# Performance work log

Measured on AMD Instinct MI355X. Metric: run time of the kernel, lower is better.

The kernel has to match this reference:

```python
import jax, jax.numpy as jnp
import numpy as np

B, C, N = 2, 29, 8192
S, K = 1024, 16  # npoint, nsample
D = C + 3


def fps(xyz_t, npoint):
    # xyz_t: [B, N, 3] -> indices [B, npoint] (furthest point sampling, starts at idx 0)
    b, n, _ = xyz_t.shape

    def step(carry, _):
        dists, farthest = carry  # [B,N], [B]
        centroid = jnp.take_along_axis(xyz_t, farthest[:, None, None], axis=1)  # [B,1,3]
        d = jnp.sum((xyz_t - centroid) ** 2, axis=-1)  # [B,N]
        dists = jnp.minimum(dists, d)
        nxt = jnp.argmax(dists, axis=-1)
        return (dists, nxt), farthest

    init = (jnp.full((b, n), 1e10, xyz_t.dtype), jnp.zeros((b,), jnp.int32))
    _, idx = jax.lax.scan(step, init, None, length=npoint)
    return jnp.transpose(idx)  # [B, npoint]


def knn_self(pts, k):
    # pts: [B, S, 3] -> k nearest neighbor indices within the same set, [B, S, k]
    sq = jnp.sum(pts * pts, axis=-1)
    d2 = sq[:, :, None] + sq[:, None, :] - 2.0 * jnp.einsum('bic,bjc->bij', pts, pts)
    _, idx = jax.lax.top_k(-d2, k)
    return idx


def group(arr, idx):
    # arr: [B, C, N], idx: [B, S, K] -> [B, C, S, K]
    return jax.vmap(lambda a, i: a[:, i])(arr, idx)


def squeeze_2x2(x):
    # RealNVP alt-order squeeze: [n, c, h, w] -> [n, 4c, h/2, w/2]
    tl = x[:, :, 0::2, 0::2]
    br = x[:, :, 1::2, 1::2]
    tr = x[:, :, 0::2, 1::2]
    bl = x[:, :, 1::2, 0::2]
    return jnp.concatenate([tl, br, tr, bl], axis=1)


def conv2d(x, w):
    return jax.lax.conv_general_dilated(
        x, w, window_strides=(1, 1), padding='VALID',
        dimension_numbers=('NCHW', 'OIHW', 'NCHW'))


def setup_inputs() -> dict:
    key = jax.random.key(0)
    ks = jax.random.split(key, 6)
    return {
        'xyz': jax.random.normal(ks[0], (B, 3, N), jnp.float32),
        'feats': jax.random.normal(ks[1], (B, C, N), jnp.float32),
        'w0': jax.random.normal(ks[2], (64, 2 * D * 4, 3, 3), jnp.float32) * 0.02,
        'w1': jax.random.normal(ks[3], (64, 64, 3, 3), jnp.float32) * 0.02,
        'w2': jax.random.normal(ks[4], (128, 64, 3, 3), jnp.float32) * 0.02,
        'w3': jax.random.normal(ks[5], (128, 128, 2, 2), jnp.float32) * 0.02,
    }


def reference(xyz, feats, w0, w1, w2, w3):
    b, c, n = feats.shape
    xyz_t = jnp.transpose(xyz, (0, 2, 1))  # [B,N,3]
    fps_idx = fps(xyz_t, S)  # [B,S]
    new_xyz = jnp.take_along_axis(xyz, fps_idx[:, None, :], axis=2)  # [B,3,S]
    new_xyz_t = jnp.transpose(new_xyz, (0, 2, 1))  # [B,S,3]
    idx = knn_self(new_xyz_t, K)  # [B,S,K], values in [0,S)

    pos_grouped = group(new_xyz, idx)  # [B,3,S,K]
    feats_grouped = group(feats, idx)  # [B,C,S,K] (indices < S, as in original)
    pos_diff = pos_grouped - new_xyz[:, :, :, None]
    fg = jnp.concatenate([pos_diff, feats_grouped], axis=1)  # [B,D,S,K]

    # pairwise outer-product features; second half ([fg;1] x [fg;1] upper block) is all ones
    outer = jnp.einsum('bdsi,bdsj->bdsij', fg, fg)  # [B,D,S,K,K]
    mat = jnp.concatenate([outer, jnp.ones_like(outer)], axis=1)  # [B,2D,S,K,K]
    mat = jnp.transpose(mat, (0, 2, 1, 3, 4)).reshape(b * S, 2 * D, K, K)
    mat = squeeze_2x2(mat)  # [B*S, 8D, K/2, K/2]

    for w in (w0, w1, w2, w3):  # use_bn=False -> Identity bns; spatial 8->6->4->2->1
        mat = jax.nn.relu(conv2d(mat, w))

    new_points = jnp.transpose(mat.reshape(b, S, -1), (0, 2, 1))  # [B,128,S]
    return new_xyz, new_points, fps_idx
```

## Files before the change

kernel.cpp:

```cpp
#include <hip/hip_runtime.h>
#include <hip/hip_bf16.h>

#pragma clang fp contract(off)

#define NPTS 8192
#define NS   1024
#define NB   2
#define NC   29
#define NK   16


__global__ __launch_bounds__(256) void prep_kernel(
    const float* __restrict__ w0, const float* __restrict__ w1,
    const float* __restrict__ w2, const float* __restrict__ w3,
    float* __restrict__ w0t, float* __restrict__ w1t,
    float* __restrict__ w2t, float* __restrict__ w3t,
    float* __restrict__ bias0)
{
    int i = blockIdx.x * 256 + threadIdx.x;
    int n = gridDim.x * 256;
    for (int e = i; e < 73728; e += n) {
        int o = e & 63, r = e >> 6, tap = r % 9, ic2 = r / 9;
        int ic = ((ic2 >> 5) << 6) + (ic2 & 31);
        w0t[e] = w0[(o * 256 + ic) * 9 + tap];
    }
    for (int e = i; e < 36864; e += n) {
        int o = e & 63, r = e >> 6, tap = r % 9, ic = r / 9;
        w1t[e] = w1[(o * 64 + ic) * 9 + tap];
    }
    for (int e = i; e < 73728; e += n) {
        int o = e & 127, r = e >> 7, tap = r % 9, ic = r / 9;
        w2t[e] = w2[(o * 64 + ic) * 9 + tap];
    }
    for (int e = i; e < 65536; e += n) {
        int o = e & 127, r = e >> 7, tap = r & 3, ic = r >> 2;
        w3t[e] = w3[(o * 128 + ic) * 4 + tap];
    }
    if (i < 64) {
        float sum = 0.0f;
        for (int q = 0; q < 4; ++q)
            for (int c = 0; c < 32; ++c)
                for (int t = 0; t < 9; ++t)
                    sum += w0[(i * 256 + q * 64 + 32 + c) * 9 + t];
        bias0[i] = sum;
    }
}

__device__ __forceinline__ float wave_max_nonneg(float x) {
    int v = __float_as_int(x);
    int t;
    t = __builtin_amdgcn_update_dpp(0, v, 0x111, 0xf, 0xf, true);
    v = __float_as_int(fmaxf(__int_as_float(v), __int_as_float(t)));
    t = __builtin_amdgcn_update_dpp(0, v, 0x112, 0xf, 0xf, true);
    v = __float_as_int(fmaxf(__int_as_float(v), __int_as_float(t)));
    t = __builtin_amdgcn_update_dpp(0, v, 0x114, 0xf, 0xf, true);
    v = __float_as_int(fmaxf(__int_as_float(v), __int_as_float(t)));
    t = __builtin_amdgcn_update_dpp(0, v, 0x118, 0xf, 0xf, true);
    v = __float_as_int(fmaxf(__int_as_float(v), __int_as_float(t)));
    t = __builtin_amdgcn_update_dpp(0, v, 0x142, 0xa, 0xf, true);
    v = __float_as_int(fmaxf(__int_as_float(v), __int_as_float(t)));
    t = __builtin_amdgcn_update_dpp(0, v, 0x143, 0xc, 0xf, true);
    v = __float_as_int(fmaxf(__int_as_float(v), __int_as_float(t)));
    return __int_as_float(__builtin_amdgcn_readlane(v, 63));
}

__global__ __launch_bounds__(1024) void fps_kernel(
    const float* __restrict__ xyz,
    float* __restrict__ nx_ws, float* __restrict__ out)
{
    int b = blockIdx.x;
    int tid = threadIdx.x;
    const float* X = xyz + b * 3 * NPTS;

    __shared__ unsigned s_max[2];
    __shared__ int s_gi[2];
    __shared__ int s_idx[NS];

    float px[8], py[8], pz[8], dist[8];
#pragma unroll
    for (int i = 0; i < 8; ++i) {
        int gi = i * 1024 + tid;
        px[i] = X[gi];
        py[i] = X[NPTS + gi];
        pz[i] = X[2 * NPTS + gi];
        dist[i] = 1e10f;
    }

    float* out_fps = out + 268288 + b * NS;
    if (tid == 0) {
        s_idx[0] = 0; out_fps[0] = 0.0f;
        s_max[0] = 0u; s_max[1] = 0u;
        s_gi[0] = 0x7fffffff; s_gi[1] = 0x7fffffff;
    }
    __syncthreads();

    float cx = X[0], cy = X[NPTS], cz = X[2 * NPTS];
    int lane = tid & 63;

    for (int it = 1; it < NS; ++it) {
        int par = it & 1;
#pragma unroll
        for (int i = 0; i < 8; ++i) {
            float dx = px[i] - cx, dy = py[i] - cy, dz = pz[i] - cz;
            float d = (dx * dx + dy * dy) + dz * dz;
            dist[i] = fminf(dist[i], d);
        }
        float m0 = fmaxf(dist[0], dist[1]);
        float m1 = fmaxf(dist[2], dist[3]);
        float m2 = fmaxf(dist[4], dist[5]);
        float m3 = fmaxf(dist[6], dist[7]);
        float m4 = fmaxf(m0, m1);
        float m5 = fmaxf(m2, m3);
        float bv = fmaxf(m4, m5);
        float wm = wave_max_nonneg(bv);
        if (lane == 0) atomicMax(&s_max[par], __float_as_uint(wm));
        __syncthreads();
        float gbv = __uint_as_float(s_max[par]);
        if (tid == 0) { s_max[par ^ 1] = 0u; s_gi[par ^ 1] = 0x7fffffff; }
        if (bv == gbv) {
            int gi = 0;
#pragma unroll
            for (int i = 7; i >= 0; --i)
                if (dist[i] == gbv) gi = (i << 10) + tid;
            atomicMin(&s_gi[par], gi);
        }
        __syncthreads();
        int idx = s_gi[par];
        if (tid == 0) { out_fps[it] = (float)idx; s_idx[it] = idx; }
        cx = X[idx]; cy = X[NPTS + idx]; cz = X[2 * NPTS + idx];
    }
    __syncthreads();
    {
        int j = s_idx[tid];
        float x = X[j], y = X[NPTS + j], z = X[2 * NPTS + j];
        nx_ws[(b * 3 + 0) * NS + tid] = x; out[(b * 3 + 0) * NS + tid] = x;
        nx_ws[(b * 3 + 1) * NS + tid] = y; out[(b * 3 + 1) * NS + tid] = y;
        nx_ws[(b * 3 + 2) * NS + tid] = z; out[(b * 3 + 2) * NS + tid] = z;
    }
}

__global__ __launch_bounds__(256) void knn_kernel(
    const float* __restrict__ nx_ws, int* __restrict__ knn_ws)
{
    int q = blockIdx.x * 4 + (threadIdx.x >> 6);
    int lane = threadIdx.x & 63;
    int b = q >> 10, s = q & 1023;
    const float* P = nx_ws + b * 3 * NS;
    float qx = P[s], qy = P[NS + s], qz = P[2 * NS + s];
    float sqq = (qx * qx + qy * qy) + qz * qz;
    int base_j = lane * 16;
    float d2[16];
    {
        const float4* x4 = (const float4*)(P + base_j);
        const float4* y4 = (const float4*)(P + NS + base_j);
        const float4* z4 = (const float4*)(P + 2 * NS + base_j);
#pragma unroll
        for (int t = 0; t < 4; ++t) {
            float4 xv = x4[t], yv = y4[t], zv = z4[t];
            float xs[4] = { xv.x, xv.y, xv.z, xv.w };
            float ys[4] = { yv.x, yv.y, yv.z, yv.w };
            float zs[4] = { zv.x, zv.y, zv.z, zv.w };
#pragma unroll
            for (int e = 0; e < 4; ++e) {
                float xj = xs[e], yj = ys[e], zj = zs[e];
                float sqj = (xj * xj + yj * yj) + zj * zj;
                float dot = (qx * xj + qy * yj) + qz * zj;
                d2[t * 4 + e] = (sqq + sqj) - 2.0f * dot;
            }
        }
    }
    for (int r = 0; r < NK; ++r) {
        float lv = 3.0e38f; int li = 0;
#pragma unroll
        for (int i = 0; i < 16; ++i) { if (d2[i] < lv) { lv = d2[i]; li = i; } }
        int gj = base_j + li;
#pragma unroll
        for (int off = 32; off > 0; off >>= 1) {
            float ov = __shfl_xor(lv, off, 64);
            int   oj = __shfl_xor(gj, off, 64);
            if (ov < lv || (ov == lv && oj < gj)) { lv = ov; gj = oj; }
        }
        if (lane == 0) knn_ws[q * NK + r] = gj;
        if ((gj >> 4) == lane) {
            int li2 = gj & 15;
#pragma unroll
            for (int i = 0; i < 16; ++i) if (i == li2) d2[i] = 3.0e38f;
        }
    }
}

template<int GODD>
__device__ __forceinline__ void conv0_accum(
    const float* __restrict__ x0r, const float* __restrict__ wbase, float acc[9])
{
    for (int ic2 = 0; ic2 < 128; ++ic2) {
        const float4* x4 = (const float4*)(x0r + ic2 * 64);
        float rr[32];
#pragma unroll
        for (int j = 0; j < 4; ++j) {
            float4 t0 = x4[j * 2], t1 = x4[j * 2 + 1];
            rr[j*8+0]=t0.x; rr[j*8+1]=t0.y; rr[j*8+2]=t0.z; rr[j*8+3]=t0.w;
            rr[j*8+4]=t1.x; rr[j*8+5]=t1.y; rr[j*8+6]=t1.z; rr[j*8+7]=t1.w;
        }
        float w[9];
#pragma unroll
        for (int t = 0; t < 9; ++t) w[t] = wbase[(ic2 * 9 + t) * 64];
#pragma unroll
        for (int pp = 0; pp < 9; ++pp) {
            const int ly = GODD ? (pp < 3 ? 0 : 1) : (pp < 6 ? 0 : 1);
            const int xx = GODD ? (pp < 3 ? pp + 3 : pp - 3) : (pp < 6 ? pp : pp - 6);
#pragma unroll
            for (int ky = 0; ky < 3; ++ky)
#pragma unroll
                for (int kx = 0; kx < 3; ++kx)
                    acc[pp] = __builtin_fmaf(w[ky * 3 + kx], rr[(ly + ky) * 8 + xx + kx], acc[pp]);
        }
    }
}

__global__ __launch_bounds__(256) void conv_kernel(
    const float* __restrict__ feats, const float* __restrict__ nx_ws,
    const int* __restrict__ knn_ws,
    const float* __restrict__ w0t, const float* __restrict__ bias0,
    const float* __restrict__ w1t, const float* __restrict__ w2t,
    const float* __restrict__ w3t, float* __restrict__ out)
{
    __shared__ float s_fg[512];
    __shared__ int   s_ni[16];
    __shared__ float s_x0[8192];
    __shared__ float s_a1[64 * 36];
    __shared__ float s_a2[64 * 16];
    __shared__ float s_a3[128 * 4];

    int bs = blockIdx.x, b = bs >> 10, s = bs & 1023;
    int tid = threadIdx.x;
    if (tid < 16) s_ni[tid] = knn_ws[bs * NK + tid];
    __syncthreads();
    const float* P = nx_ws + b * 3 * NS;
#pragma unroll
    for (int e = tid; e < 512; e += 256) {
        int d = e >> 4, k = e & 15; int j = s_ni[k];
        float v = (d < 3) ? (P[d * NS + j] - P[d * NS + s])
                          : feats[(b * NC + (d - 3)) * NPTS + j];
        s_fg[e] = v;
    }
    __syncthreads();
    for (int e = tid; e < 8192; e += 256) {
        int ic2 = e >> 6, pos = e & 63, u = pos >> 3, v = pos & 7;
        int q = ic2 >> 5, ch = ic2 & 31;
        int ro = q & 1, co = ((q + 1) >> 1) & 1;
        s_x0[e] = s_fg[ch * 16 + 2 * u + ro] * s_fg[ch * 16 + 2 * v + co];
    }
    __syncthreads();

    int o = tid & 63, g = tid >> 6;
    {
        int r0 = g + (g >> 1);
        float acc[9];
        float bz = bias0[o];
#pragma unroll
        for (int p = 0; p < 9; ++p) acc[p] = bz;
        const float* x0r = s_x0 + r0 * 8;
        const float* wb = w0t + o;
        if (g & 1) conv0_accum<1>(x0r, wb, acc);
        else       conv0_accum<0>(x0r, wb, acc);
#pragma unroll
        for (int pp = 0; pp < 9; ++pp) s_a1[o * 36 + g * 9 + pp] = fmaxf(acc[pp], 0.0f);
    }
    __syncthreads();
    {
        float a[4] = {0, 0, 0, 0};
        const float* wb = w1t + o;
        for (int ic = 0; ic < 64; ++ic) {
            const float2* ar2 = (const float2*)(s_a1 + ic * 36 + g * 6);
            float r[18];
#pragma unroll
            for (int t = 0; t < 9; ++t) { float2 tv = ar2[t]; r[t*2] = tv.x; r[t*2+1] = tv.y; }
            float w[9];
#pragma unroll
            for (int t = 0; t < 9; ++t) w[t] = wb[(ic * 9 + t) * 64];
#pragma unroll
            for (int x = 0; x < 4; ++x)
#pragma unroll
                for (int ky = 0; ky < 3; ++ky)
#pragma unroll
                    for (int kx = 0; kx < 3; ++kx)
                        a[x] = __builtin_fmaf(w[ky * 3 + kx], r[ky * 6 + x + kx], a[x]);
        }
#pragma unroll
        for (int x = 0; x < 4; ++x) s_a2[o * 16 + g * 4 + x] = fmaxf(a[x], 0.0f);
    }
    __syncthreads();
    {
        int o2 = tid & 127, g2 = tid >> 7;
        float a[2] = {0, 0};
        const float* wb = w2t + o2;
        for (int ic = 0; ic < 64; ++ic) {
            const float4* ar4 = (const float4*)(s_a2 + ic * 16 + g2 * 4);
            float r[12];
#pragma unroll
            for (int t = 0; t < 3; ++t) { float4 tv = ar4[t]; r[t*4]=tv.x; r[t*4+1]=tv.y; r[t*4+2]=tv.z; r[t*4+3]=tv.w; }
            float w[9];
#pragma unroll
            for (int t = 0; t < 9; ++t) w[t] = wb[(ic * 9 + t) * 128];
#pragma unroll
            for (int x = 0; x < 2; ++x)
#pragma unroll
                for (int ky = 0; ky < 3; ++ky)
#pragma unroll
                    for (int kx = 0; kx < 3; ++kx)
                        a[x] = __builtin_fmaf(w[ky * 3 + kx], r[ky * 4 + x + kx], a[x]);
        }
#pragma unroll
        for (int x = 0; x < 2; ++x) s_a3[o2 * 4 + g2 * 2 + x] = fmaxf(a[x], 0.0f);
    }
    __syncthreads();
    if (tid < 128) {
        float acc = 0.0f;
        const float* wb = w3t + tid;
        for (int ic = 0; ic < 128; ++ic) {
            float4 av = *(const float4*)(s_a3 + ic * 4);
            float wa = wb[(ic * 4 + 0) * 128];
            float wbv = wb[(ic * 4 + 1) * 128];
            float wc = wb[(ic * 4 + 2) * 128];
            float wd = wb[(ic * 4 + 3) * 128];
            acc = __builtin_fmaf(wa, av.x, acc);
            acc = __builtin_fmaf(wbv, av.y, acc);
            acc = __builtin_fmaf(wc, av.z, acc);
            acc = __builtin_fmaf(wd, av.w, acc);
        }
        out[6144 + (b * 128 + tid) * NS + s] = fmaxf(acc, 0.0f);
    }
}

extern "C" void kernel_launch(void* const* d_in, const int* in_sizes, int n_in,
                              void* d_out, int out_size, void* d_ws, size_t ws_size,
                              hipStream_t stream) {
    const float* xyz   = (const float*)d_in[0];
    const float* feats = (const float*)d_in[1];
    const float* w0    = (const float*)d_in[2];
    const float* w1    = (const float*)d_in[3];
    const float* w2    = (const float*)d_in[4];
    const float* w3    = (const float*)d_in[5];
    float* out = (float*)d_out;

    char* ws = (char*)d_ws;
    float* nx_ws  = (float*)(ws + 8192);
    int*   knn_ws = (int*)(ws + 32768);
    float* w0t    = (float*)(ws + 163840);
    float* bias0  = (float*)(ws + 458752);
    float* w1t    = (float*)(ws + 459008);
    float* w2t    = (float*)(ws + 606464);
    float* w3t    = (float*)(ws + 901376);

    prep_kernel<<<128, 256, 0, stream>>>(w0, w1, w2, w3, w0t, w1t, w2t, w3t, bias0);
    fps_kernel<<<NB, 1024, 0, stream>>>(xyz, nx_ws, out);
    knn_kernel<<<(NB * NS) / 4, 256, 0, stream>>>(nx_ws, knn_ws);
    conv_kernel<<<NB * NS, 256, 0, stream>>>(feats, nx_ws, knn_ws, w0t, bias0, w1t, w2t, w3t, out);
}
```

Before: 1.447 ms.

## Restructure FPS with packed 64-bit argmax key and single barrier per iteration

The furthest-point-sampling kernel now uses 256 threads, each holding 32 points as float2 vectors, where it used 1024 threads with 8 points each. The two-phase max-then-min-index reduction, which needed two barriers per iteration, is replaced by one 64-bit atomicMax on a key packing the distance with the inverted index. A per-iteration slot array removes the need to reset shared state. This targets barrier and atomic latency in the serial 1023-step loop. The cost is more per-thread work and higher register pressure.

```diff
diff --git a/kernel.cpp b/kernel.cpp
--- a/kernel.cpp
+++ b/kernel.cpp
@@ -64,78 +64,82 @@
     return __int_as_float(__builtin_amdgcn_readlane(v, 63));
 }
 
-__global__ __launch_bounds__(1024) void fps_kernel(
+typedef float v2f __attribute__((ext_vector_type(2)));
+
+__global__ __launch_bounds__(256, 1) void fps_kernel(
     const float* __restrict__ xyz,
     float* __restrict__ nx_ws, float* __restrict__ out)
 {
     int b = blockIdx.x;
     int tid = threadIdx.x;
+    int lane = tid & 63;
     const float* X = xyz + b * 3 * NPTS;
 
-    __shared__ unsigned s_max[2];
-    __shared__ int s_gi[2];
-    __shared__ int s_idx[NS];
-
-    float px[8], py[8], pz[8], dist[8];
-#pragma unroll
-    for (int i = 0; i < 8; ++i) {
-        int gi = i * 1024 + tid;
-        px[i] = X[gi];
-        py[i] = X[NPTS + gi];
-        pz[i] = X[2 * NPTS + gi];
-        dist[i] = 1e10f;
+    __shared__ unsigned long long s_key[NS];
+
+    v2f px[16], py[16], pz[16], dist[16];
+
+    for (int i = tid; i < NS; i += 256) s_key[i] = 0ull;
+    if (tid == 0) s_key[0] = 0xFFFFFFFFull;
+
+#pragma unroll
+    for (int i = 0; i < 16; ++i) {
+        int g2 = i * 512 + tid * 2;
+        px[i] = *(const v2f*)(X + g2);
+        py[i] = *(const v2f*)(X + NPTS + g2);
+        pz[i] = *(const v2f*)(X + 2 * NPTS + g2);
+        dist[i] = (v2f){1e10f, 1e10f};
+    }
+    __syncthreads();
+
+    float cx = X[0], cy = X[NPTS], cz = X[2 * NPTS];
+
+    for (int it = 1; it < NS; ++it) {
+        v2f c2x = {cx, cx}, c2y = {cy, cy}, c2z = {cz, cz};
+#pragma unroll
+        for (int i = 0; i < 16; ++i) {
+            v2f dx = px[i] - c2x, dy = py[i] - c2y, dz = pz[i] - c2z;
+            v2f d = (dx * dx + dy * dy) + dz * dz;
+            v2f dd = dist[i];
+            dd.x = fminf(dd.x, d.x);
+            dd.y = fminf(dd.y, d.y);
+            dist[i] = dd;
+        }
+        float t16[16];
+#pragma unroll
+        for (int i = 0; i < 16; ++i) t16[i] = fmaxf(dist[i].x, dist[i].y);
+        float t8[8];
+#pragma unroll
+        for (int i = 0; i < 8; ++i) t8[i] = fmaxf(t16[2 * i], t16[2 * i + 1]);
+        float t4[4];
+#pragma unroll
+        for (int i = 0; i < 4; ++i) t4[i] = fmaxf(t8[2 * i], t8[2 * i + 1]);
+        float bv = fmaxf(fmaxf(t4[0], t4[1]), fmaxf(t4[2], t4[3]));
+        float wm = wave_max_nonneg(bv);
+        if (bv == wm) {
+            int gi = 0;
+#pragma unroll
+            for (int i = 15; i >= 0; --i) {
+                if (dist[i].y == wm) gi = i * 512 + tid * 2 + 1;
+                if (dist[i].x == wm) gi = i * 512 + tid * 2;
+            }
+            unsigned long long key =
+                ((unsigned long long)__float_as_uint(wm) << 32) | (unsigned)(~gi);
+            atomicMax(&s_key[it], key);
+        }
+        __syncthreads();
+        int idx = (int)(~(unsigned)s_key[it]);
+        cx = X[idx]; cy = X[NPTS + idx]; cz = X[2 * NPTS + idx];
     }
 
     float* out_fps = out + 268288 + b * NS;
-    if (tid == 0) {
-        s_idx[0] = 0; out_fps[0] = 0.0f;
-        s_max[0] = 0u; s_max[1] = 0u;
-        s_gi[0] = 0x7fffffff; s_gi[1] = 0x7fffffff;
-    }
-    __syncthreads();
-
-    float cx = X[0], cy = X[NPTS], cz = X[2 * NPTS];
-    int lane = tid & 63;
-
-    for (int it = 1; it < NS; ++it) {
-        int par = it & 1;
-#pragma unroll
-        for (int i = 0; i < 8; ++i) {
-            float dx = px[i] - cx, dy = py[i] - cy, dz = pz[i] - cz;
-            float d = (dx * dx + dy * dy) + dz * dz;
-            dist[i] = fminf(dist[i], d);
-        }
-        float m0 = fmaxf(dist[0], dist[1]);
-        float m1 = fmaxf(dist[2], dist[3]);
-        float m2 = fmaxf(dist[4], dist[5]);
-        float m3 = fmaxf(dist[6], dist[7]);
-        float m4 = fmaxf(m0, m1);
-        float m5 = fmaxf(m2, m3);
-        float bv = fmaxf(m4, m5);
-        float wm = wave_max_nonneg(bv);
-        if (lane == 0) atomicMax(&s_max[par], __float_as_uint(wm));
-        __syncthreads();
-        float gbv = __uint_as_float(s_max[par]);
-        if (tid == 0) { s_max[par ^ 1] = 0u; s_gi[par ^ 1] = 0x7fffffff; }
-        if (bv == gbv) {
-            int gi = 0;
-#pragma unroll
-            for (int i = 7; i >= 0; --i)
-                if (dist[i] == gbv) gi = (i << 10) + tid;
-            atomicMin(&s_gi[par], gi);
-        }
-        __syncthreads();
-        int idx = s_gi[par];
-        if (tid == 0) { out_fps[it] = (float)idx; s_idx[it] = idx; }
-        cx = X[idx]; cy = X[NPTS + idx]; cz = X[2 * NPTS + idx];
-    }
-    __syncthreads();
-    {
-        int j = s_idx[tid];
+    for (int i = tid; i < NS; i += 256) {
+        int j = (int)(~(unsigned)s_key[i]);
+        out_fps[i] = (float)j;
         float x = X[j], y = X[NPTS + j], z = X[2 * NPTS + j];
-        nx_ws[(b * 3 + 0) * NS + tid] = x; out[(b * 3 + 0) * NS + tid] = x;
-        nx_ws[(b * 3 + 1) * NS + tid] = y; out[(b * 3 + 1) * NS + tid] = y;
-        nx_ws[(b * 3 + 2) * NS + tid] = z; out[(b * 3 + 2) * NS + tid] = z;
+        nx_ws[(b * 3 + 0) * NS + i] = x; out[(b * 3 + 0) * NS + i] = x;
+        nx_ws[(b * 3 + 1) * NS + i] = y; out[(b * 3 + 1) * NS + i] = y;
+        nx_ws[(b * 3 + 2) * NS + i] = z; out[(b * 3 + 2) * NS + i] = z;
     }
 }
 
@@ -354,7 +358,7 @@
     float* w3t    = (float*)(ws + 901376);
 
     prep_kernel<<<128, 256, 0, stream>>>(w0, w1, w2, w3, w0t, w1t, w2t, w3t, bias0);
-    fps_kernel<<<NB, 1024, 0, stream>>>(xyz, nx_ws, out);
+    fps_kernel<<<NB, 256, 0, stream>>>(xyz, nx_ws, out);
     knn_kernel<<<(NB * NS) / 4, 256, 0, stream>>>(nx_ws, knn_ws);
     conv_kernel<<<NB * NS, 256, 0, stream>>>(feats, nx_ws, knn_ws, w0t, bias0, w1t, w2t, w3t, out);
 }
```

Result: slower. 1.720 ms (+18.9%).

## Fuse FPS argmax into single packed 64-bit atomic, halving barriers per iteration

Applied to the files above, without the earlier changes.

Replaces the two-phase block argmax in the FPS loop (atomicMax on the value, barrier, atomicMin on the index, barrier) with a single 64-bit atomicMax on a key packing the distance bits and the inverted index. Each iteration writes into its own shared slot, so no reset is needed and only one __syncthreads remains per step. The final index array is recovered from the keys afterwards. This halves barrier count on the serial 1023-iteration critical path, at the cost of 64-bit LDS atomics, where every wave's candidate lanes now contend on the shared slot.

```diff
diff --git a/kernel.cpp b/kernel.cpp
--- a/kernel.cpp
+++ b/kernel.cpp
@@ -72,9 +72,7 @@
     int tid = threadIdx.x;
     const float* X = xyz + b * 3 * NPTS;
 
-    __shared__ unsigned s_max[2];
-    __shared__ int s_gi[2];
-    __shared__ int s_idx[NS];
+    __shared__ unsigned long long s_key[NS];
 
     float px[8], py[8], pz[8], dist[8];
 #pragma unroll
@@ -85,20 +83,18 @@
         pz[i] = X[2 * NPTS + gi];
         dist[i] = 1e10f;
     }
-
-    float* out_fps = out + 268288 + b * NS;
-    if (tid == 0) {
-        s_idx[0] = 0; out_fps[0] = 0.0f;
-        s_max[0] = 0u; s_max[1] = 0u;
-        s_gi[0] = 0x7fffffff; s_gi[1] = 0x7fffffff;
-    }
+#pragma unroll
+    for (int i = 0; i < 8; ++i) {
+        asm volatile("" : "+v"(px[i]), "+v"(py[i]), "+v"(pz[i]));
+    }
+
+    s_key[tid] = 0ull;
+    if (tid == 0) s_key[0] = 0xFFFFFFFFull;
     __syncthreads();
 
     float cx = X[0], cy = X[NPTS], cz = X[2 * NPTS];
-    int lane = tid & 63;
 
     for (int it = 1; it < NS; ++it) {
-        int par = it & 1;
 #pragma unroll
         for (int i = 0; i < 8; ++i) {
             float dx = px[i] - cx, dy = py[i] - cy, dz = pz[i] - cz;
@@ -109,29 +105,26 @@
         float m1 = fmaxf(dist[2], dist[3]);
         float m2 = fmaxf(dist[4], dist[5]);
         float m3 = fmaxf(dist[6], dist[7]);
-        float m4 = fmaxf(m0, m1);
-        float m5 = fmaxf(m2, m3);
-        float bv = fmaxf(m4, m5);
+        float bv = fmaxf(fmaxf(m0, m1), fmaxf(m2, m3));
         float wm = wave_max_nonneg(bv);
-        if (lane == 0) atomicMax(&s_max[par], __float_as_uint(wm));
+        if (bv == wm) {
+            int gi = 0;
+#pragma unroll
+            for (int i = 7; i >= 0; --i)
+                if (dist[i] == wm) gi = (i << 10) + tid;
+            unsigned long long key =
+                ((unsigned long long)__float_as_uint(wm) << 32) | (unsigned)(~gi);
+            atomicMax(&s_key[it], key);
+        }
         __syncthreads();
-        float gbv = __uint_as_float(s_max[par]);
-        if (tid == 0) { s_max[par ^ 1] = 0u; s_gi[par ^ 1] = 0x7fffffff; }
-        if (bv == gbv) {
-            int gi = 0;
-#pragma unroll
-            for (int i = 7; i >= 0; --i)
-                if (dist[i] == gbv) gi = (i << 10) + tid;
-            atomicMin(&s_gi[par], gi);
-        }
-        __syncthreads();
-        int idx = s_gi[par];
-        if (tid == 0) { out_fps[it] = (float)idx; s_idx[it] = idx; }
+        int idx = __builtin_amdgcn_readfirstlane((int)(~(unsigned)s_key[it]));
         cx = X[idx]; cy = X[NPTS + idx]; cz = X[2 * NPTS + idx];
     }
-    __syncthreads();
-    {
-        int j = s_idx[tid];
+
+    float* out_fps = out + 268288 + b * NS;
+    {
+        int j = (int)(~(unsigned)s_key[tid]);
+        out_fps[tid] = (float)j;
         float x = X[j], y = X[NPTS + j], z = X[2 * NPTS + j];
         nx_ws[(b * 3 + 0) * NS + tid] = x; out[(b * 3 + 0) * NS + tid] = x;
         nx_ws[(b * 3 + 1) * NS + tid] = y; out[(b * 3 + 1) * NS + tid] = y;
```

After: 1.463 ms. Within noise of the previous version (+1.1%).
